# Kernel tuning notes

Hardware: AMD Instinct MI355X
Metric: run time of the kernel (lower is better)

The kernel has to match this reference:

```python
import jax, jax.numpy as jnp
import numpy as np
from jax import lax


def setup_inputs() -> dict:
    key = jax.random.key(0)
    k1, k2, k3, k4 = jax.random.split(key, 4)
    N, D, B, R, EF = 100000, 256, 64, 32, 32
    storage = jax.random.normal(k1, (N, D), dtype=jnp.float32)
    query = jax.random.normal(k2, (B, D), dtype=jnp.float32)
    graph = jax.random.randint(k3, (N, R), 0, N, dtype=jnp.int32)      # fixed-degree NSW adjacency
    initial = jax.random.randint(k4, (B, EF), 0, N, dtype=jnp.int32)   # random entry points (entry())
    return {"query": query, "storage": storage, "graph": graph,
            "initial": initial, "k": 10, "ef_search": EF}


def reference(query, storage, graph, initial, k, ef_search):
    """Batched greedy best-first NSW search (ef_search fixed expansion steps)."""
    N = storage.shape[0]
    INF = jnp.float32(1e30)

    def sqdist(q, ids):
        diff = storage[ids] - q            # [R, D] gather
        return jnp.sum(diff * diff, axis=-1)

    def search_one(q, init):
        cd = sqdist(q, init)                               # candidate distances [EF]
        visited = jnp.zeros((N,), jnp.bool_).at[init].set(True)
        expanded = jnp.zeros((N,), jnp.bool_)

        def step(state, _):
            cid, cd, visited, expanded = state
            # pick closest unexpanded candidate
            pickd = jnp.where(expanded[cid], INF, cd)
            j = jnp.argmin(pickd)
            u = cid[j]
            expanded = expanded.at[u].set(True)
            # expand neighbors of u
            nbrs = graph[u]                                # [R]
            fresh = ~visited[nbrs]
            nd = jnp.where(fresh, sqdist(q, nbrs), INF)    # skip already-visited
            visited = visited.at[nbrs].set(True)
            # merge candidate pool, keep ef_search best
            all_ids = jnp.concatenate([cid, nbrs])
            all_d = jnp.concatenate([cd, nd])
            negd, idx = lax.top_k(-all_d, ef_search)
            return (all_ids[idx], -negd, visited, expanded), None

        (cid, cd, _, _), _ = lax.scan(step, (init, cd, visited, expanded),
                                      None, length=ef_search)
        negk, idx = lax.top_k(-cd, k)
        return cid[idx], -negk

    topk_ids, topk_dists = jax.vmap(search_one)(query, initial)
    return topk_ids, topk_dists
```

## Files before the change

kernel.cpp:

```cpp
#include <hip/hip_runtime.h>


#define DIMS   256
#define RDEG   32
#define EFPOOL 32
#define KOUT   10
#define NWORDS 3125
#define INF_D  1e30f

typedef unsigned long long u64;

__global__ __launch_bounds__(64, 1) void nsw_wave_kernel(
    const float* __restrict__ query,
    const float* __restrict__ storage,
    const int*   __restrict__ graph,
    const int*   __restrict__ initial,
    float*       __restrict__ out,
    int B)
{
    __shared__ unsigned int visited[NWORDS];
    __shared__ unsigned int expanded[NWORDS];
    __shared__ float4 qsh[DIMS / 4];
    __shared__ u64    keys[64];
    __shared__ float  sc_d[EFPOOL];
    __shared__ int    sc_id[EFPOOL];

    const int l    = threadIdx.x;
    const int b    = blockIdx.x;
    const int nb   = l & 31;
    const int half = l >> 5;

    for (int i = l; i < NWORDS; i += 64) { visited[i] = 0u; expanded[i] = 0u; }

    qsh[l] = reinterpret_cast<const float4*>(query + (size_t)b * DIMS)[l];

    float pool_d  = INF_D;
    int   pool_id = 0;
    int   u       = 0;
    int   nbid    = initial[b * EFPOOL + nb];

    if (l < 32) atomicOr(&visited[nbid >> 5], 1u << (nbid & 31));

    float4 r[32];
    {
        const float4* sp = reinterpret_cast<const float4*>(
            storage + (size_t)nbid * DIMS) + half * 32;
        #pragma unroll
        for (int j = 0; j < 32; ++j) r[j] = sp[j];
    }

    for (int s = 0; s <= EFPOOL; ++s) {
        if (s > 0 && l == 0) expanded[u >> 5] |= 1u << (u & 31);

        bool fresh = true;
        if (s > 0) {
            unsigned vw = visited[nbid >> 5];
            fresh = !((vw >> (nbid & 31)) & 1u);
            if ((l < 32) && fresh) atomicOr(&visited[nbid >> 5], 1u << (nbid & 31));
        }

        bool ounexp = !((expanded[pool_id >> 5] >> (pool_id & 31)) & 1u);
        u64  obm    = __ballot(ounexp && (l < 32));
        int  oslot  = (obm == 0ull) ? 0 : (__ffsll(obm) - 1);
        float old_d = __shfl(pool_d,  oslot, 64);
        int   old_id= __shfl(pool_id, oslot, 64);
        bool  old_ok= (obm != 0ull);

        float a0 = 0.f, a1 = 0.f, a2 = 0.f, a3 = 0.f;
        #pragma unroll
        for (int j = 0; j < 32; ++j) {
            float4 q = qsh[half * 32 + j];
            float d0 = r[j].x - q.x; a0 = fmaf(d0, d0, a0);
            float d1 = r[j].y - q.y; a1 = fmaf(d1, d1, a1);
            float d2 = r[j].z - q.z; a2 = fmaf(d2, d2, a2);
            float d3 = r[j].w - q.w; a3 = fmaf(d3, d3, a3);
        }
        float part = (a0 + a1) + (a2 + a3);
        float d  = part + __shfl_xor(part, 32, 64);
        float nd = fresh ? d : INF_D;

        int nnbid = nbid;
        int uspec = 0;
        if (s < EFPOOL) {
            u64 nk = fresh ? (((u64)__float_as_uint(nd) << 6) | (u64)(32 + nb))
                           : ~0ull;
            #pragma unroll
            for (int m = 1; m < 64; m <<= 1) {
                u64 o = __shfl_xor(nk, m, 64);
                nk = (o < nk) ? o : nk;
            }
            int new_id = __shfl(nbid, ((int)(nk & 63) - 32) & 31, 64);
            u64 ok = old_ok ? (((u64)__float_as_uint(old_d) << 6) | (u64)oslot)
                            : ~0ull;
            uspec = (ok < nk) ? old_id : new_id;
            nnbid = graph[(size_t)uspec * RDEG + nb];
        }

        {
            float ed  = half ? nd   : pool_d;
            int   eid = half ? nbid : pool_id;
            u64 key = ((u64)__float_as_uint(ed) << 6) | (unsigned)l;
            keys[l] = key;
            int rank = 0;
            #pragma unroll
            for (int j = 0; j < 64; ++j)
                rank += (keys[j] < key) ? 1 : 0;
            if (rank < EFPOOL) { sc_d[rank] = ed; sc_id[rank] = eid; }
            pool_d  = sc_d[nb];
            pool_id = sc_id[nb];
        }

        if (s < EFPOOL) {
            bool unexp = !((expanded[pool_id >> 5] >> (pool_id & 31)) & 1u);
            u64 bm = __ballot(unexp && (l < 32));
            int slot = (bm == 0ull) ? 0 : (__ffsll(bm) - 1);
            int utrue = sc_id[slot];
            int ut = __builtin_amdgcn_readfirstlane(utrue);
            int us = __builtin_amdgcn_readfirstlane(uspec);
            if (ut != us)
                nnbid = graph[(size_t)utrue * RDEG + nb];
            u    = utrue;
            nbid = nnbid;
            const float4* sp = reinterpret_cast<const float4*>(
                storage + (size_t)nbid * DIMS) + half * 32;
            #pragma unroll
            for (int j = 0; j < 32; ++j) r[j] = sp[j];
        }
    }

    if (l < KOUT) {
        out[b * KOUT + l]            = (float)pool_id;
        out[B * KOUT + b * KOUT + l] = pool_d;
    }
}

extern "C" void kernel_launch(void* const* d_in, const int* in_sizes, int n_in,
                              void* d_out, int out_size, void* d_ws, size_t ws_size,
                              hipStream_t stream) {
    const float* query   = (const float*)d_in[0];
    const float* storage = (const float*)d_in[1];
    const int*   graph   = (const int*)d_in[2];
    const int*   initial = (const int*)d_in[3];
    float* out = (float*)d_out;

    const int B = in_sizes[0] / DIMS;

    nsw_wave_kernel<<<B, 64, 0, stream>>>(query, storage, graph, initial, out, B);
}
```

Baseline: 228.2 us.

## Defer pool merge off critical path and prefetch graph row for old candidate

Moves the 64-entry rank-sort merge of the candidate pool to the start of the next iteration, so the next node is chosen directly from the min of the old best candidate and the new neighbours without waiting for the sort. It also issues the graph row load for the best old unexpanded candidate early, so it overlaps the distance computation. The intent is a shorter serial dependency chain per expansion step: graph load, then storage gather. It relies on a more subtle selection rule that must still match the reference, including the case where no old candidate is unexpanded, and it adds a final merge after the loop.

```diff
diff --git a/kernel.cpp b/kernel.cpp
--- a/kernel.cpp
+++ b/kernel.cpp
@@ -38,6 +38,8 @@
     int   pool_id = 0;
     int   u       = 0;
     int   nbid    = initial[b * EFPOOL + nb];
+    float pend_nd = INF_D;
+    int   pend_nbid = 0;
 
     if (l < 32) atomicOr(&visited[nbid >> 5], 1u << (nbid & 31));
 
@@ -50,7 +52,20 @@
     }
 
     for (int s = 0; s <= EFPOOL; ++s) {
-        if (s > 0 && l == 0) expanded[u >> 5] |= 1u << (u & 31);
+        if (s > 0) {
+            if (l == 0) expanded[u >> 5] |= 1u << (u & 31);
+            float ed  = half ? pend_nd   : pool_d;
+            int   eid = half ? pend_nbid : pool_id;
+            u64 key = ((u64)__float_as_uint(ed) << 6) | (unsigned)l;
+            keys[l] = key;
+            int rank = 0;
+            #pragma unroll
+            for (int j = 0; j < 64; ++j)
+                rank += (keys[j] < key) ? 1 : 0;
+            if (rank < EFPOOL) { sc_d[rank] = ed; sc_id[rank] = eid; }
+            pool_d  = sc_d[nb];
+            pool_id = sc_id[nb];
+        }
 
         bool fresh = true;
         if (s > 0) {
@@ -65,6 +80,12 @@
         float old_d = __shfl(pool_d,  oslot, 64);
         int   old_id= __shfl(pool_id, oslot, 64);
         bool  old_ok= (obm != 0ull);
+        float d31   = __shfl(pool_d, 31, 64);
+        int   gpre  = 0;
+        if (s < EFPOOL) {
+            gpre = graph[(size_t)old_id * RDEG + nb];
+            asm volatile("" : "+v"(gpre));
+        }
 
         float a0 = 0.f, a1 = 0.f, a2 = 0.f, a3 = 0.f;
         #pragma unroll
@@ -79,53 +100,46 @@
         float d  = part + __shfl_xor(part, 32, 64);
         float nd = fresh ? d : INF_D;
 
-        int nnbid = nbid;
-        int uspec = 0;
         if (s < EFPOOL) {
             u64 nk = fresh ? (((u64)__float_as_uint(nd) << 6) | (u64)(32 + nb))
                            : ~0ull;
             #pragma unroll
-            for (int m = 1; m < 64; m <<= 1) {
+            for (int m = 1; m < 32; m <<= 1) {
                 u64 o = __shfl_xor(nk, m, 64);
                 nk = (o < nk) ? o : nk;
             }
-            int new_id = __shfl(nbid, ((int)(nk & 63) - 32) & 31, 64);
-            u64 ok = old_ok ? (((u64)__float_as_uint(old_d) << 6) | (u64)oslot)
-                            : ~0ull;
-            uspec = (ok < nk) ? old_id : new_id;
-            nnbid = graph[(size_t)uspec * RDEG + nb];
-        }
-
-        {
-            float ed  = half ? nd   : pool_d;
-            int   eid = half ? nbid : pool_id;
-            u64 key = ((u64)__float_as_uint(ed) << 6) | (unsigned)l;
-            keys[l] = key;
-            int rank = 0;
-            #pragma unroll
-            for (int j = 0; j < 64; ++j)
-                rank += (keys[j] < key) ? 1 : 0;
-            if (rank < EFPOOL) { sc_d[rank] = ed; sc_id[rank] = eid; }
-            pool_d  = sc_d[nb];
-            pool_id = sc_id[nb];
-        }
-
-        if (s < EFPOOL) {
-            bool unexp = !((expanded[pool_id >> 5] >> (pool_id & 31)) & 1u);
-            u64 bm = __ballot(unexp && (l < 32));
-            int slot = (bm == 0ull) ? 0 : (__ffsll(bm) - 1);
-            int utrue = sc_id[slot];
-            int ut = __builtin_amdgcn_readfirstlane(utrue);
-            int us = __builtin_amdgcn_readfirstlane(uspec);
-            if (ut != us)
-                nnbid = graph[(size_t)utrue * RDEG + nb];
-            u    = utrue;
-            nbid = nnbid;
+            int wslot  = ((int)(nk & 63) - 32) & 31;
+            int new_id = __shfl(nbid, wslot, 64);
+            u64 okey = old_ok ? (((u64)__float_as_uint(old_d) << 6) | (u64)oslot)
+                              : ~0ull;
+            float dnew = __uint_as_float((unsigned)(nk >> 6));
+            bool oldpath = (!(nk < okey)) || (!old_ok && !(dnew < d31));
+            u = oldpath ? old_id : new_id;
+            int nn = oldpath ? gpre
+                             : graph[(size_t)new_id * RDEG + nb];
+            pend_nd = nd; pend_nbid = nbid;
+            nbid = nn;
             const float4* sp = reinterpret_cast<const float4*>(
                 storage + (size_t)nbid * DIMS) + half * 32;
             #pragma unroll
             for (int j = 0; j < 32; ++j) r[j] = sp[j];
+        } else {
+            pend_nd = nd; pend_nbid = nbid;
         }
+    }
+
+    {
+        float ed  = half ? pend_nd   : pool_d;
+        int   eid = half ? pend_nbid : pool_id;
+        u64 key = ((u64)__float_as_uint(ed) << 6) | (unsigned)l;
+        keys[l] = key;
+        int rank = 0;
+        #pragma unroll
+        for (int j = 0; j < 64; ++j)
+            rank += (keys[j] < key) ? 1 : 0;
+        if (rank < EFPOOL) { sc_d[rank] = ed; sc_id[rank] = eid; }
+        pool_d  = sc_d[nb];
+        pool_id = sc_id[nb];
     }
 
     if (l < KOUT) {
```

Result: no change. 230.1 us (+0.8%).
